# Kernel tuning notes

Hardware: AMD Instinct MI355X
Metric: run time of the kernel (lower is better)

The kernel has to match this reference:

```python
import jax, jax.numpy as jnp
import numpy as np

N = 100000   # nodes per type (author == paper count here)
E = 800000   # edges per edge type
D = 128      # input feature dim
HID = 128    # hidden_channels
OUT = 64     # out_channels
L = 2        # num_layers


def setup_inputs() -> dict:
    key = jax.random.key(0)
    ks = jax.random.split(key, 14)
    x_author = jax.random.normal(ks[0], (N, D), jnp.float32)
    x_paper = jax.random.normal(ks[1], (N, D), jnp.float32)
    edge_ap = jnp.stack([
        jax.random.randint(ks[2], (E,), 0, N),
        jax.random.randint(ks[3], (E,), 0, N),
    ]).astype(jnp.int32)  # [2,E] author->paper (src,dst)
    # paper->author: ensure every paper id appears as a source so the
    # meta-path conversion keeps all E edges (static shape under jit)
    pa_src = jnp.concatenate([jnp.arange(N), jax.random.randint(ks[4], (E - N,), 0, N)]).astype(jnp.int32)
    pa_dst = jax.random.randint(ks[5], (E,), 0, N).astype(jnp.int32)
    edge_pa = jnp.stack([pa_src, pa_dst])
    perm = jax.random.permutation(ks[6], N).astype(jnp.int32)  # DGI corruption
    s = 0.05
    # SAGEConv params: [layer, edge_type] with edge_type 0 = (author->paper), 1 = (paper->author)
    sage_Wl = jax.random.normal(ks[7], (L, 2, HID, D), jnp.float32) * s   # neighbor lin
    sage_Wr = jax.random.normal(ks[8], (L, 2, HID, D), jnp.float32) * s   # root lin
    sage_b = jnp.zeros((L, 2, HID), jnp.float32)
    # GATConv (heads=1) params
    gat_W = jax.random.normal(ks[9], (OUT, HID), jnp.float32) * s
    gat_att_src = jax.random.normal(ks[10], (OUT,), jnp.float32) * s
    gat_att_dst = jax.random.normal(ks[11], (OUT,), jnp.float32) * s
    gat_b = jnp.zeros((OUT,), jnp.float32)
    prelu_a = jnp.asarray(0.25, jnp.float32)
    return dict(x_author=x_author, x_paper=x_paper, sage_Wl=sage_Wl, sage_Wr=sage_Wr,
                sage_b=sage_b, gat_W=gat_W, gat_att_src=gat_att_src, gat_att_dst=gat_att_dst,
                gat_b=gat_b, prelu_a=prelu_a, edge_ap=edge_ap, edge_pa=edge_pa, perm=perm)


def _sage(x_src, x_dst, src, dst, Wl, Wr, b, n_dst):
    # SAGEConv: mean-aggregate neighbor feats, lin_l(agg) + lin_r(root) + bias
    agg = jax.ops.segment_sum(x_src[src], dst, num_segments=n_dst)       # [n_dst, D]
    cnt = jax.ops.segment_sum(jnp.ones((src.shape[0],), x_src.dtype), dst, num_segments=n_dst)
    mean = agg / jnp.maximum(cnt, 1.0)[:, None]
    return mean @ Wl.T + x_dst @ Wr.T + b


def _gat_prelu(feat, src, dst, W, a_src, a_dst, b, prelu_a, n):
    # GATConv heads=1 (self loops already appended by caller) + PReLU
    h = feat @ W.T                                                        # [n, OUT]
    e = jax.nn.leaky_relu((h @ a_src)[src] + (h @ a_dst)[dst], 0.2)       # [E']
    m = jax.ops.segment_max(e, dst, num_segments=n)
    ex = jnp.exp(e - m[dst])
    den = jax.ops.segment_sum(ex, dst, num_segments=n)
    coef = ex / den[dst]
    out = jax.ops.segment_sum(coef[:, None] * h[src], dst, num_segments=n) + b
    return jnp.where(out >= 0, out, prelu_a * out)


def reference(x_author, x_paper, sage_Wl, sage_Wr, sage_b, gat_W, gat_att_src,
              gat_att_dst, gat_b, prelu_a, edge_ap, edge_pa, perm):
    # Original loop feeds xx_dict into every layer, so only the LAST layer's
    # output survives; and only x_dict['author'] is consumed downstream.
    l = L - 1
    h_author = jax.nn.leaky_relu(
        _sage(x_paper, x_author, edge_pa[0], edge_pa[1],
              sage_Wl[l, 1], sage_Wr[l, 1], sage_b[l, 1], N), 0.01)
    # meta-path author->author edges (paper mapped via last-write paper->author dict)
    p2a = jnp.zeros((N,), jnp.int32).at[edge_pa[0]].set(edge_pa[1])
    self_loop = jnp.arange(N, dtype=jnp.int32)  # GATConv add_self_loops=True
    meta_src = jnp.concatenate([edge_ap[0], self_loop])
    meta_dst = jnp.concatenate([p2a[edge_ap[1]], self_loop])
    pos = _gat_prelu(h_author, meta_src, meta_dst, gat_W, gat_att_src, gat_att_dst, gat_b, prelu_a, N)
    neg = _gat_prelu(h_author[perm], meta_src, meta_dst, gat_W, gat_att_src, gat_att_dst, gat_b, prelu_a, N)
    summary = jnp.mean(pos, axis=0)
    return pos, neg, summary
```

## Files before the change

kernel.cpp:

```cpp
#include <hip/hip_runtime.h>
#include <stdint.h>

#define NN 100000
#define EE 800000
#define DD 128
#define HH 128
#define OO 64

#define SPA 40
#define SME 112

#define PREP_EDGE_B  3125
#define PREP_CASTX_B 12500
#define PREP_CASTW_B 40
#define P2_SAGE_B    25000
#define P2_CMP_B     391
#define P3_GEMM_B    782
#define P3_META_B    3125

typedef __attribute__((ext_vector_type(8))) short short8v;
typedef __attribute__((ext_vector_type(4))) float f32x4;

__device__ __forceinline__ unsigned short f2bf(float f) {
    union { float f; unsigned int u; } v; v.f = f;
    unsigned int u = v.u;
    u = (u + 0x7fffu + ((u >> 16) & 1u)) >> 16;
    return (unsigned short)u;
}
__device__ __forceinline__ float bf2f(unsigned short b) {
    union { unsigned int u; float f; } v; v.u = ((unsigned int)b) << 16;
    return v.f;
}

__global__ __launch_bounds__(256) void k_prep(const int* __restrict__ pa_src,
                                              const int* __restrict__ pa_dst,
                                              const float* __restrict__ x,
                                              const float* __restrict__ Wl,
                                              const float* __restrict__ Wr,
                                              const float* __restrict__ Wg,
                                              int* __restrict__ amax,
                                              int* __restrict__ cnt_pa,
                                              int* __restrict__ col_pa,
                                              unsigned short* __restrict__ xbf,
                                              unsigned short* __restrict__ wbf) {
    int b = blockIdx.x, t = threadIdx.x;
    if (b < PREP_EDGE_B) {
        int e = b * 256 + t;
        if (e >= EE) return;
        int s = pa_src[e], d = pa_dst[e];
        atomicMax(&amax[s], e);
        int pos = atomicAdd(&cnt_pa[d], 1);
        if (pos < SPA) __builtin_nontemporal_store(s, &col_pa[d * SPA + pos]);
    } else if (b < PREP_EDGE_B + PREP_CASTX_B) {
        long i = (long)(b - PREP_EDGE_B) * 256 + t;
        if (i >= (long)NN * DD / 4) return;
        float4 v = ((const float4*)x)[i];
        ushort4 w;
        w.x = f2bf(v.x); w.y = f2bf(v.y); w.z = f2bf(v.z); w.w = f2bf(v.w);
        ((ushort4*)xbf)[i] = w;
    } else {
        int i4 = (b - PREP_EDGE_B - PREP_CASTX_B) * 256 + t;
        if (i4 >= 10240) return;
        float4 v;
        if (i4 < 4096)       v = ((const float4*)Wl)[i4];
        else if (i4 < 8192)  v = ((const float4*)Wr)[i4 - 4096];
        else                 v = ((const float4*)Wg)[i4 - 8192];
        ushort4 w;
        w.x = f2bf(v.x); w.y = f2bf(v.y); w.z = f2bf(v.z); w.w = f2bf(v.w);
        ((ushort4*)wbf)[i4] = w;
    }
}

__global__ __launch_bounds__(256) void k_pack2(const int* __restrict__ cnt_pa,
                                               const int* __restrict__ col_pa,
                                               const unsigned short* __restrict__ xbf,
                                               const int* __restrict__ amax,
                                               const int* __restrict__ pa_dst,
                                               int* __restrict__ p2a32,
                                               unsigned short* __restrict__ mean_bf) {
    int b = blockIdx.x, t = threadIdx.x;
    if (b < P2_SAGE_B) {
        long gid = (long)b * 256 + t;
        int d = (int)(gid >> 6);
        if (d >= NN) return;
        int lane = (int)(gid & 63);
        int dcnt = cnt_pa[d];
        int deg = (dcnt > SPA) ? SPA : dcnt;
        const int* row = col_pa + d * SPA;
        float ax = 0.f, ay = 0.f;
        int i = 0;
        for (; i + 3 < deg; i += 4) {
            int s0 = row[i], s1 = row[i + 1], s2 = row[i + 2], s3 = row[i + 3];
            ushort2 v0 = ((const ushort2*)(xbf + (long)s0 * DD))[lane];
            ushort2 v1 = ((const ushort2*)(xbf + (long)s1 * DD))[lane];
            ushort2 v2 = ((const ushort2*)(xbf + (long)s2 * DD))[lane];
            ushort2 v3 = ((const ushort2*)(xbf + (long)s3 * DD))[lane];
            ax += (bf2f(v0.x) + bf2f(v1.x)) + (bf2f(v2.x) + bf2f(v3.x));
            ay += (bf2f(v0.y) + bf2f(v1.y)) + (bf2f(v2.y) + bf2f(v3.y));
        }
        for (; i < deg; ++i) {
            int s = row[i];
            ushort2 v = ((const ushort2*)(xbf + (long)s * DD))[lane];
            ax += bf2f(v.x);
            ay += bf2f(v.y);
        }
        float sc = 1.0f / fmaxf((float)dcnt, 1.0f);
        ushort2 w;
        w.x = f2bf(ax * sc);
        w.y = f2bf(ay * sc);
        ((ushort2*)(mean_bf + (long)d * DD))[lane] = w;
    } else {
        int s = (b - P2_SAGE_B) * 256 + t;
        if (s >= NN) return;
        p2a32[s] = pa_dst[amax[s]];
    }
}

__global__ __launch_bounds__(256) void k_pack3(const unsigned short* __restrict__ mean_bf,
                                               const float* __restrict__ xa,
                                               const unsigned short* __restrict__ wbf,
                                               const float* __restrict__ sb,
                                               const float* __restrict__ asrc,
                                               const float* __restrict__ adst,
                                               unsigned short* __restrict__ hg,
                                               float* __restrict__ al_s,
                                               float* __restrict__ al_d,
                                               const int* __restrict__ ap_src,
                                               const int* __restrict__ ap_dst,
                                               const int* __restrict__ p2a32,
                                               int* __restrict__ cnt_meta,
                                               int* __restrict__ col_meta) {
    __shared__ unsigned short hs[4 * 32 * 128];
    int b = blockIdx.x, t = threadIdx.x;
    if (b >= P3_GEMM_B) {
        int e = (b - P3_GEMM_B) * 256 + t;
        if (e >= EE) return;
        int d = p2a32[ap_dst[e]];
        int pos = atomicAdd(&cnt_meta[d], 1);
        if (pos < SME) __builtin_nontemporal_store(ap_src[e], &col_meta[d * SME + pos]);
        return;
    }
    const unsigned short* wl = wbf;
    const unsigned short* wr = wbf + 16384;
    const unsigned short* wg = wbf + 32768;
    int wave = t >> 6, lane = t & 63;
    int rowbase = b * 128 + wave * 32;
    int lr = lane & 15;
    int q = lane >> 4;
    int kq = q * 8;
    int r0 = rowbase + lr, r1 = r0 + 16;
    int cr0 = (r0 < NN) ? r0 : 0;
    int cr1 = (r1 < NN) ? r1 : 0;

    f32x4 acc[2][8];
    #pragma unroll
    for (int i = 0; i < 2; ++i)
        #pragma unroll
        for (int j = 0; j < 8; ++j) { f32x4 z = {0.f,0.f,0.f,0.f}; acc[i][j] = z; }

    #pragma unroll
    for (int k0 = 0; k0 < DD; k0 += 32) {
        int kk = k0 + kq;
        short8v am0 = *(const short8v*)(mean_bf + (long)cr0 * DD + kk);
        short8v am1 = *(const short8v*)(mean_bf + (long)cr1 * DD + kk);
        const float4* q0 = (const float4*)(xa + (long)cr0 * DD + kk);
        const float4* q1 = (const float4*)(xa + (long)cr1 * DD + kk);
        float4 a0 = q0[0], b0 = q0[1], a1 = q1[0], b1 = q1[1];
        short8v ax0, ax1;
        ax0[0]=(short)f2bf(a0.x); ax0[1]=(short)f2bf(a0.y); ax0[2]=(short)f2bf(a0.z); ax0[3]=(short)f2bf(a0.w);
        ax0[4]=(short)f2bf(b0.x); ax0[5]=(short)f2bf(b0.y); ax0[6]=(short)f2bf(b0.z); ax0[7]=(short)f2bf(b0.w);
        ax1[0]=(short)f2bf(a1.x); ax1[1]=(short)f2bf(a1.y); ax1[2]=(short)f2bf(a1.z); ax1[3]=(short)f2bf(a1.w);
        ax1[4]=(short)f2bf(b1.x); ax1[5]=(short)f2bf(b1.y); ax1[6]=(short)f2bf(b1.z); ax1[7]=(short)f2bf(b1.w);
        #pragma unroll
        for (int nb = 0; nb < 8; ++nb) {
            int o = nb * 16 + lr;
            short8v bl = *(const short8v*)(wl + o * DD + kk);
            short8v br = *(const short8v*)(wr + o * DD + kk);
            acc[0][nb] = __builtin_amdgcn_mfma_f32_16x16x32_bf16(am0, bl, acc[0][nb], 0, 0, 0);
            acc[1][nb] = __builtin_amdgcn_mfma_f32_16x16x32_bf16(am1, bl, acc[1][nb], 0, 0, 0);
            acc[0][nb] = __builtin_amdgcn_mfma_f32_16x16x32_bf16(ax0, br, acc[0][nb], 0, 0, 0);
            acc[1][nb] = __builtin_amdgcn_mfma_f32_16x16x32_bf16(ax1, br, acc[1][nb], 0, 0, 0);
        }
    }
    char* hbase = (char*)hs + wave * 8192;
    #pragma unroll
    for (int rh = 0; rh < 2; ++rh) {
        #pragma unroll
        for (int nb = 0; nb < 8; ++nb) {
            int col = nb * 16 + lr;
            float bias = sb[col];
            #pragma unroll
            for (int r = 0; r < 4; ++r) {
                int lrow = rh * 16 + q * 4 + r;
                float v = acc[rh][nb][r] + bias;
                v = (v >= 0.f) ? v : 0.01f * v;
                int boff = (lrow * 256 + col * 2) ^ ((lrow & 7) << 4);
                *(unsigned short*)(hbase + boff) = f2bf(v);
            }
        }
    }
    f32x4 acc2[2][4];
    #pragma unroll
    for (int i = 0; i < 2; ++i)
        #pragma unroll
        for (int j = 0; j < 4; ++j) { f32x4 z = {0.f,0.f,0.f,0.f}; acc2[i][j] = z; }

    #pragma unroll
    for (int k0 = 0; k0 < HH; k0 += 32) {
        int kk = k0 + kq;
        int boff0 = (lr * 256 + kk * 2) ^ ((lr & 7) << 4);
        int boff1 = ((16 + lr) * 256 + kk * 2) ^ ((lr & 7) << 4);
        short8v a0 = *(const short8v*)(hbase + boff0);
        short8v a1 = *(const short8v*)(hbase + boff1);
        #pragma unroll
        for (int nb = 0; nb < 4; ++nb) {
            short8v bg = *(const short8v*)(wg + (nb * 16 + lr) * HH + kk);
            acc2[0][nb] = __builtin_amdgcn_mfma_f32_16x16x32_bf16(a0, bg, acc2[0][nb], 0, 0, 0);
            acc2[1][nb] = __builtin_amdgcn_mfma_f32_16x16x32_bf16(a1, bg, acc2[1][nb], 0, 0, 0);
        }
    }
    float a_s[4], a_d[4];
    #pragma unroll
    for (int nb = 0; nb < 4; ++nb) { a_s[nb] = asrc[nb * 16 + lr]; a_d[nb] = adst[nb * 16 + lr]; }
    #pragma unroll
    for (int rh = 0; rh < 2; ++rh) {
        float ss[4] = {0.f,0.f,0.f,0.f}, dd[4] = {0.f,0.f,0.f,0.f};
        #pragma unroll
        for (int nb = 0; nb < 4; ++nb) {
            #pragma unroll
            for (int r = 0; r < 4; ++r) {
                int row = rowbase + rh * 16 + q * 4 + r;
                unsigned short wb = f2bf(acc2[rh][nb][r]);
                if (row < NN) hg[(long)row * OO + nb * 16 + lr] = wb;
                float w = bf2f(wb);
                ss[r] += w * a_s[nb];
                dd[r] += w * a_d[nb];
            }
        }
        #pragma unroll
        for (int r = 0; r < 4; ++r) {
            float s = ss[r], dv = dd[r];
            #pragma unroll
            for (int off = 1; off < 16; off <<= 1) {
                s  += __shfl_xor(s,  off, 64);
                dv += __shfl_xor(dv, off, 64);
            }
            int row = rowbase + rh * 16 + q * 4 + r;
            if (lr == 0 && row < NN) { al_s[row] = s; al_d[row] = dv; }
        }
    }
}

__global__ __launch_bounds__(256) void k_gat_gather(const int* __restrict__ cnt_meta,
                                                    const int* __restrict__ col_meta,
                                                    const int* __restrict__ perm,
                                                    const float* __restrict__ al_s,
                                                    const float* __restrict__ al_d,
                                                    const unsigned short* __restrict__ hg,
                                                    const float* __restrict__ gb,
                                                    const float* __restrict__ prelu_a,
                                                    float* __restrict__ out) {
    long gid = (long)blockIdx.x * 256 + threadIdx.x;
    int d = (int)(gid >> 6);
    if (d >= NN) return;
    int j = (int)(gid & 63);
    int deg = cnt_meta[d];
    if (deg > SME) deg = SME;
    const int* row = col_meta + d * SME;
    int pd = perm[d];
    float add = al_d[d];
    float adn = al_d[pd];
    float lp = al_s[d] + add;   lp = (lp >= 0.f) ? lp : 0.2f * lp;
    float ln = al_s[pd] + adn;  ln = (ln >= 0.f) ? ln : 0.2f * ln;
    float xps = __expf(lp), xns = __expf(ln);
    float denp = xps, denn = xns;
    float accp = xps * bf2f(hg[((long)d << 6) + j]);
    float accn = xns * bf2f(hg[((long)pd << 6) + j]);

    for (int base = 0; base < deg; base += 64) {
        int cnt = deg - base;
        if (cnt > 64) cnt = 64;
        int s = 0, ps = 0;
        float xp = 0.f, xn = 0.f;
        if (j < cnt) {
            s = row[base + j];
            ps = perm[s];
            float l0 = al_s[s] + add;   l0 = (l0 >= 0.f) ? l0 : 0.2f * l0;
            xp = __expf(l0);
            float m0 = al_s[ps] + adn;  m0 = (m0 >= 0.f) ? m0 : 0.2f * m0;
            xn = __expf(m0);
        }
        float tp = xp, tn = xn;
        #pragma unroll
        for (int off = 32; off; off >>= 1) {
            tp += __shfl_xor(tp, off, 64);
            tn += __shfl_xor(tn, off, 64);
        }
        denp += tp;
        denn += tn;
        int e = 0;
        for (; e + 3 < cnt; e += 4) {
            int s0 = __shfl(s, e),   s1 = __shfl(s, e + 1),   s2 = __shfl(s, e + 2),   s3 = __shfl(s, e + 3);
            int p0 = __shfl(ps, e),  p1 = __shfl(ps, e + 1),  p2 = __shfl(ps, e + 2),  p3 = __shfl(ps, e + 3);
            float a0 = __shfl(xp, e), a1 = __shfl(xp, e + 1), a2 = __shfl(xp, e + 2), a3 = __shfl(xp, e + 3);
            float b0 = __shfl(xn, e), b1 = __shfl(xn, e + 1), b2 = __shfl(xn, e + 2), b3 = __shfl(xn, e + 3);
            float h0 = bf2f(hg[((long)s0 << 6) + j]);
            float h1 = bf2f(hg[((long)s1 << 6) + j]);
            float h2 = bf2f(hg[((long)s2 << 6) + j]);
            float h3 = bf2f(hg[((long)s3 << 6) + j]);
            float g0 = bf2f(hg[((long)p0 << 6) + j]);
            float g1 = bf2f(hg[((long)p1 << 6) + j]);
            float g2 = bf2f(hg[((long)p2 << 6) + j]);
            float g3 = bf2f(hg[((long)p3 << 6) + j]);
            accp += (a0 * h0 + a1 * h1) + (a2 * h2 + a3 * h3);
            accn += (b0 * g0 + b1 * g1) + (b2 * g2 + b3 * g3);
        }
        for (; e < cnt; ++e) {
            int sb2 = __shfl(s, e);
            int pb = __shfl(ps, e);
            float ab = __shfl(xp, e);
            float bb = __shfl(xn, e);
            accp += ab * bf2f(hg[((long)sb2 << 6) + j]);
            accn += bb * bf2f(hg[((long)pb << 6) + j]);
        }
    }
    float bias = gb[j];
    float a = prelu_a[0];
    float vp = accp / denp + bias;
    vp = (vp >= 0.f) ? vp : a * vp;
    out[((long)d << 6) + j] = vp;
    float vn = accn / denn + bias;
    vn = (vn >= 0.f) ? vn : a * vn;
    out[((long)(NN + d) << 6) + j] = vn;
}

__global__ __launch_bounds__(256) void k_summary(const float* __restrict__ out_pos,
                                                 float* __restrict__ summary) {
    int t = threadIdx.x;
    int j = t & 63, sub = t >> 6;
    float acc = 0.f;
    for (int row = blockIdx.x * 4 + sub; row < NN; row += 256 * 4) {
        acc += out_pos[(long)row * OO + j];
    }
    __shared__ float red[4][OO];
    red[sub][j] = acc;
    __syncthreads();
    if (sub == 0) {
        float ttl = red[0][j] + red[1][j] + red[2][j] + red[3][j];
        atomicAdd(summary + j, ttl * (1.0f / NN));
    }
}

extern "C" void kernel_launch(void* const* d_in, const int* in_sizes, int n_in,
                              void* d_out, int out_size, void* d_ws, size_t ws_size,
                              hipStream_t stream) {
    const float* x_author = (const float*)d_in[0];
    const float* x_paper  = (const float*)d_in[1];
    const float* sage_Wl  = (const float*)d_in[2];
    const float* sage_Wr  = (const float*)d_in[3];
    const float* sage_b   = (const float*)d_in[4];
    const float* gat_W    = (const float*)d_in[5];
    const float* gat_as   = (const float*)d_in[6];
    const float* gat_ad   = (const float*)d_in[7];
    const float* gat_b    = (const float*)d_in[8];
    const float* prelu_a  = (const float*)d_in[9];
    const int*   edge_ap  = (const int*)d_in[10];
    const int*   edge_pa  = (const int*)d_in[11];
    const int*   perm     = (const int*)d_in[12];

    char* ws = (char*)d_ws;
    int*   cnt_pa    = (int*)(ws + 0);
    int*   cnt_meta  = (int*)(ws + 400000);
    int*   amax      = (int*)(ws + 800000);
    int*   p2a32     = (int*)(ws + 1200000);
    float* al_s      = (float*)(ws + 1600000);
    float* al_d      = (float*)(ws + 2000000);
    unsigned short* wbf = (unsigned short*)(ws + 2400000);
    int*   col_pa    = (int*)(ws + 2481920);
    unsigned short* mean_bf = (unsigned short*)(ws + 18481920);
    unsigned short* xbf     = (unsigned short*)(ws + 44081920);
    int*   col_meta  = (int*)(ws + 44081920);
    unsigned short* hg = (unsigned short*)col_pa;

    hipMemsetAsync(d_ws, 0, 1200000, stream);
    hipMemsetAsync((char*)d_out + (size_t)2 * NN * OO * sizeof(float), 0,
                   OO * sizeof(float), stream);

    const float* Wl = sage_Wl + 3 * HH * DD;
    const float* Wr = sage_Wr + 3 * HH * DD;
    const float* sb = sage_b  + 3 * HH;

    k_prep<<<PREP_EDGE_B + PREP_CASTX_B + PREP_CASTW_B, 256, 0, stream>>>(
        edge_pa, edge_pa + EE, x_paper, Wl, Wr, gat_W, amax, cnt_pa, col_pa, xbf, wbf);
    k_pack2<<<P2_SAGE_B + P2_CMP_B, 256, 0, stream>>>(
        cnt_pa, col_pa, xbf, amax, edge_pa + EE, p2a32, mean_bf);
    k_pack3<<<P3_GEMM_B + P3_META_B, 256, 0, stream>>>(
        mean_bf, x_author, wbf, sb, gat_as, gat_ad, hg, al_s, al_d,
        edge_ap, edge_ap + EE, p2a32, cnt_meta, col_meta);
    k_gat_gather<<<(NN * 64 + 255) / 256, 256, 0, stream>>>(cnt_meta, col_meta, perm,
                                                            al_s, al_d, hg, gat_b, prelu_a,
                                                            (float*)d_out);
    k_summary<<<256, 256, 0, stream>>>((float*)d_out, (float*)d_out + 2L * NN * OO);
}
```

Measured before the change: 339.4 us.

## Replace materialized meta-path CSR with two-level author-paper adjacency walk

Rather than building a bucketed author->author meta-path adjacency with atomics after the paper->author map exists, the edges are bucketed by paper in the prep kernel, in parallel with the paper->author bucketing. The pack kernel then builds an inverse map from each author to the papers that resolve to it. The GAT gather walks those papers and their author lists. This removes the 800k-edge atomic scatter that sat in the GEMM kernel and lets the GEMM run alone. The cost is a nested loop in the gather that handles only about 8 edges per 64-lane pass, which leaves many lanes idle, and extra workspace memory.

```diff
diff --git a/kernel.cpp b/kernel.cpp
--- a/kernel.cpp
+++ b/kernel.cpp
@@ -8,15 +8,15 @@
 #define OO 64
 
 #define SPA 40
-#define SME 112
-
-#define PREP_EDGE_B  3125
+#define SAP 40
+#define SIV 24
+
+#define PREP_PAIR_B  6250
 #define PREP_CASTX_B 12500
 #define PREP_CASTW_B 40
 #define P2_SAGE_B    25000
-#define P2_CMP_B     391
-#define P3_GEMM_B    782
-#define P3_META_B    3125
+#define P2_INV_B     391
+#define GEMM_B       782
 
 typedef __attribute__((ext_vector_type(8))) short short8v;
 typedef __attribute__((ext_vector_type(4))) float f32x4;
@@ -34,6 +34,8 @@
 
 __global__ __launch_bounds__(256) void k_prep(const int* __restrict__ pa_src,
                                               const int* __restrict__ pa_dst,
+                                              const int* __restrict__ ap_src,
+                                              const int* __restrict__ ap_dst,
                                               const float* __restrict__ x,
                                               const float* __restrict__ Wl,
                                               const float* __restrict__ Wr,
@@ -41,25 +43,33 @@
                                               int* __restrict__ amax,
                                               int* __restrict__ cnt_pa,
                                               int* __restrict__ col_pa,
+                                              int* __restrict__ cnt_ap,
+                                              int* __restrict__ col_ap,
                                               unsigned short* __restrict__ xbf,
                                               unsigned short* __restrict__ wbf) {
     int b = blockIdx.x, t = threadIdx.x;
-    if (b < PREP_EDGE_B) {
-        int e = b * 256 + t;
+    if (b < PREP_PAIR_B) {
+        int e = (b >> 1) * 256 + t;
         if (e >= EE) return;
-        int s = pa_src[e], d = pa_dst[e];
-        atomicMax(&amax[s], e);
-        int pos = atomicAdd(&cnt_pa[d], 1);
-        if (pos < SPA) __builtin_nontemporal_store(s, &col_pa[d * SPA + pos]);
-    } else if (b < PREP_EDGE_B + PREP_CASTX_B) {
-        long i = (long)(b - PREP_EDGE_B) * 256 + t;
+        if ((b & 1) == 0) {
+            int s = pa_src[e], d = pa_dst[e];
+            atomicMax(&amax[s], e);
+            int pos = atomicAdd(&cnt_pa[d], 1);
+            if (pos < SPA) __builtin_nontemporal_store(s, &col_pa[d * SPA + pos]);
+        } else {
+            int s = ap_src[e], p = ap_dst[e];
+            int pos = atomicAdd(&cnt_ap[p], 1);
+            if (pos < SAP) __builtin_nontemporal_store(s, &col_ap[p * SAP + pos]);
+        }
+    } else if (b < PREP_PAIR_B + PREP_CASTX_B) {
+        long i = (long)(b - PREP_PAIR_B) * 256 + t;
         if (i >= (long)NN * DD / 4) return;
         float4 v = ((const float4*)x)[i];
         ushort4 w;
         w.x = f2bf(v.x); w.y = f2bf(v.y); w.z = f2bf(v.z); w.w = f2bf(v.w);
         ((ushort4*)xbf)[i] = w;
     } else {
-        int i4 = (b - PREP_EDGE_B - PREP_CASTX_B) * 256 + t;
+        int i4 = (b - PREP_PAIR_B - PREP_CASTX_B) * 256 + t;
         if (i4 >= 10240) return;
         float4 v;
         if (i4 < 4096)       v = ((const float4*)Wl)[i4];
@@ -76,7 +86,8 @@
                                                const unsigned short* __restrict__ xbf,
                                                const int* __restrict__ amax,
                                                const int* __restrict__ pa_dst,
-                                               int* __restrict__ p2a32,
+                                               int* __restrict__ cnt_inv,
+                                               int* __restrict__ col_inv,
                                                unsigned short* __restrict__ mean_bf) {
     int b = blockIdx.x, t = threadIdx.x;
     if (b < P2_SAGE_B) {
@@ -110,36 +121,25 @@
         w.y = f2bf(ay * sc);
         ((ushort2*)(mean_bf + (long)d * DD))[lane] = w;
     } else {
-        int s = (b - P2_SAGE_B) * 256 + t;
-        if (s >= NN) return;
-        p2a32[s] = pa_dst[amax[s]];
-    }
-}
-
-__global__ __launch_bounds__(256) void k_pack3(const unsigned short* __restrict__ mean_bf,
-                                               const float* __restrict__ xa,
-                                               const unsigned short* __restrict__ wbf,
-                                               const float* __restrict__ sb,
-                                               const float* __restrict__ asrc,
-                                               const float* __restrict__ adst,
-                                               unsigned short* __restrict__ hg,
-                                               float* __restrict__ al_s,
-                                               float* __restrict__ al_d,
-                                               const int* __restrict__ ap_src,
-                                               const int* __restrict__ ap_dst,
-                                               const int* __restrict__ p2a32,
-                                               int* __restrict__ cnt_meta,
-                                               int* __restrict__ col_meta) {
+        int p = (b - P2_SAGE_B) * 256 + t;
+        if (p >= NN) return;
+        int d = pa_dst[amax[p]];
+        int pos = atomicAdd(&cnt_inv[d], 1);
+        if (pos < SIV) col_inv[d * SIV + pos] = p;
+    }
+}
+
+__global__ __launch_bounds__(256) void k_gemm(const unsigned short* __restrict__ mean_bf,
+                                              const float* __restrict__ xa,
+                                              const unsigned short* __restrict__ wbf,
+                                              const float* __restrict__ sb,
+                                              const float* __restrict__ asrc,
+                                              const float* __restrict__ adst,
+                                              unsigned short* __restrict__ hg,
+                                              float* __restrict__ al_s,
+                                              float* __restrict__ al_d) {
     __shared__ unsigned short hs[4 * 32 * 128];
     int b = blockIdx.x, t = threadIdx.x;
-    if (b >= P3_GEMM_B) {
-        int e = (b - P3_GEMM_B) * 256 + t;
-        if (e >= EE) return;
-        int d = p2a32[ap_dst[e]];
-        int pos = atomicAdd(&cnt_meta[d], 1);
-        if (pos < SME) __builtin_nontemporal_store(ap_src[e], &col_meta[d * SME + pos]);
-        return;
-    }
     const unsigned short* wl = wbf;
     const unsigned short* wr = wbf + 16384;
     const unsigned short* wg = wbf + 32768;
@@ -251,8 +251,10 @@
     }
 }
 
-__global__ __launch_bounds__(256) void k_gat_gather(const int* __restrict__ cnt_meta,
-                                                    const int* __restrict__ col_meta,
+__global__ __launch_bounds__(256) void k_gat_gather(const int* __restrict__ cnt_inv,
+                                                    const int* __restrict__ col_inv,
+                                                    const int* __restrict__ cnt_ap,
+                                                    const int* __restrict__ col_ap,
                                                     const int* __restrict__ perm,
                                                     const float* __restrict__ al_s,
                                                     const float* __restrict__ al_d,
@@ -264,9 +266,8 @@
     int d = (int)(gid >> 6);
     if (d >= NN) return;
     int j = (int)(gid & 63);
-    int deg = cnt_meta[d];
-    if (deg > SME) deg = SME;
-    const int* row = col_meta + d * SME;
+    int npap = cnt_inv[d];
+    if (npap > SIV) npap = SIV;
     int pd = perm[d];
     float add = al_d[d];
     float adn = al_d[pd];
@@ -277,13 +278,15 @@
     float accp = xps * bf2f(hg[((long)d << 6) + j]);
     float accn = xns * bf2f(hg[((long)pd << 6) + j]);
 
-    for (int base = 0; base < deg; base += 64) {
-        int cnt = deg - base;
-        if (cnt > 64) cnt = 64;
+    for (int ip = 0; ip < npap; ++ip) {
+        int p = col_inv[d * SIV + ip];
+        int na = cnt_ap[p];
+        if (na > SAP) na = SAP;
+        const int* arow = col_ap + p * SAP;
         int s = 0, ps = 0;
         float xp = 0.f, xn = 0.f;
-        if (j < cnt) {
-            s = row[base + j];
+        if (j < na) {
+            s = arow[j];
             ps = perm[s];
             float l0 = al_s[s] + add;   l0 = (l0 >= 0.f) ? l0 : 0.2f * l0;
             xp = __expf(l0);
@@ -299,7 +302,7 @@
         denp += tp;
         denn += tn;
         int e = 0;
-        for (; e + 3 < cnt; e += 4) {
+        for (; e + 3 < na; e += 4) {
             int s0 = __shfl(s, e),   s1 = __shfl(s, e + 1),   s2 = __shfl(s, e + 2),   s3 = __shfl(s, e + 3);
             int p0 = __shfl(ps, e),  p1 = __shfl(ps, e + 1),  p2 = __shfl(ps, e + 2),  p3 = __shfl(ps, e + 3);
             float a0 = __shfl(xp, e), a1 = __shfl(xp, e + 1), a2 = __shfl(xp, e + 2), a3 = __shfl(xp, e + 3);
@@ -315,7 +318,7 @@
             accp += (a0 * h0 + a1 * h1) + (a2 * h2 + a3 * h3);
             accn += (b0 * g0 + b1 * g1) + (b2 * g2 + b3 * g3);
         }
-        for (; e < cnt; ++e) {
+        for (; e < na; ++e) {
             int sb2 = __shfl(s, e);
             int pb = __shfl(ps, e);
             float ab = __shfl(xp, e);
@@ -370,19 +373,20 @@
 
     char* ws = (char*)d_ws;
     int*   cnt_pa    = (int*)(ws + 0);
-    int*   cnt_meta  = (int*)(ws + 400000);
-    int*   amax      = (int*)(ws + 800000);
-    int*   p2a32     = (int*)(ws + 1200000);
+    int*   cnt_ap    = (int*)(ws + 400000);
+    int*   cnt_inv   = (int*)(ws + 800000);
+    int*   amax      = (int*)(ws + 1200000);
     float* al_s      = (float*)(ws + 1600000);
     float* al_d      = (float*)(ws + 2000000);
     unsigned short* wbf = (unsigned short*)(ws + 2400000);
     int*   col_pa    = (int*)(ws + 2481920);
-    unsigned short* mean_bf = (unsigned short*)(ws + 18481920);
+    int*   col_ap    = (int*)(ws + 18481920);
+    int*   col_inv   = (int*)(ws + 34481920);
     unsigned short* xbf     = (unsigned short*)(ws + 44081920);
-    int*   col_meta  = (int*)(ws + 44081920);
+    unsigned short* mean_bf = (unsigned short*)(ws + 69681920);
     unsigned short* hg = (unsigned short*)col_pa;
 
-    hipMemsetAsync(d_ws, 0, 1200000, stream);
+    hipMemsetAsync(d_ws, 0, 1600000, stream);
     hipMemsetAsync((char*)d_out + (size_t)2 * NN * OO * sizeof(float), 0,
                    OO * sizeof(float), stream);
 
@@ -390,15 +394,15 @@
     const float* Wr = sage_Wr + 3 * HH * DD;
     const float* sb = sage_b  + 3 * HH;
 
-    k_prep<<<PREP_EDGE_B + PREP_CASTX_B + PREP_CASTW_B, 256, 0, stream>>>(
-        edge_pa, edge_pa + EE, x_paper, Wl, Wr, gat_W, amax, cnt_pa, col_pa, xbf, wbf);
-    k_pack2<<<P2_SAGE_B + P2_CMP_B, 256, 0, stream>>>(
-        cnt_pa, col_pa, xbf, amax, edge_pa + EE, p2a32, mean_bf);
-    k_pack3<<<P3_GEMM_B + P3_META_B, 256, 0, stream>>>(
-        mean_bf, x_author, wbf, sb, gat_as, gat_ad, hg, al_s, al_d,
-        edge_ap, edge_ap + EE, p2a32, cnt_meta, col_meta);
-    k_gat_gather<<<(NN * 64 + 255) / 256, 256, 0, stream>>>(cnt_meta, col_meta, perm,
-                                                            al_s, al_d, hg, gat_b, prelu_a,
+    k_prep<<<PREP_PAIR_B + PREP_CASTX_B + PREP_CASTW_B, 256, 0, stream>>>(
+        edge_pa, edge_pa + EE, edge_ap, edge_ap + EE, x_paper, Wl, Wr, gat_W,
+        amax, cnt_pa, col_pa, cnt_ap, col_ap, xbf, wbf);
+    k_pack2<<<P2_SAGE_B + P2_INV_B, 256, 0, stream>>>(
+        cnt_pa, col_pa, xbf, amax, edge_pa + EE, cnt_inv, col_inv, mean_bf);
+    k_gemm<<<GEMM_B, 256, 0, stream>>>(mean_bf, x_author, wbf, sb, gat_as, gat_ad,
+                                       hg, al_s, al_d);
+    k_gat_gather<<<(NN * 64 + 255) / 256, 256, 0, stream>>>(cnt_inv, col_inv, cnt_ap, col_ap,
+                                                            perm, al_s, al_d, hg, gat_b, prelu_a,
                                                             (float*)d_out);
     k_summary<<<256, 256, 0, stream>>>((float*)d_out, (float*)d_out + 2L * NN * OO);
 }
```

New measurement: 410.3 us. 1.21x slower.

## Drop p2a buffer and interleave meta-edge build with SAGE gather

Applied to the files above, without the earlier changes.

Removes the intermediate p2a32 array: the meta-edge bucketing now resolves the paper-to-author mapping inline via pa_dst[amax[p]]. When the workspace is large enough, col_meta gets its own region so the meta bucketing can run in the same launch as the SAGE mean gather, with one meta block interleaved every 9 blocks. The GEMM then runs alone in its own kernel. The aim is to overlap the atomic-heavy meta build with the bandwidth-bound gather and shorten the GEMM launch. The cost is an extra dependent load per edge and a path that depends on workspace size.

```diff
diff --git a/kernel.cpp b/kernel.cpp
--- a/kernel.cpp
+++ b/kernel.cpp
@@ -13,10 +13,9 @@
 #define PREP_EDGE_B  3125
 #define PREP_CASTX_B 12500
 #define PREP_CASTW_B 40
-#define P2_SAGE_B    25000
-#define P2_CMP_B     391
-#define P3_GEMM_B    782
-#define P3_META_B    3125
+#define SAGE_B       25000
+#define META_B       3125
+#define GEMM_B       782
 
 typedef __attribute__((ext_vector_type(8))) short short8v;
 typedef __attribute__((ext_vector_type(4))) float f32x4;
@@ -30,6 +29,55 @@
 __device__ __forceinline__ float bf2f(unsigned short b) {
     union { unsigned int u; float f; } v; v.u = ((unsigned int)b) << 16;
     return v.f;
+}
+
+__device__ __forceinline__ void sage_body(long gid,
+                                          const int* __restrict__ cnt_pa,
+                                          const int* __restrict__ col_pa,
+                                          const unsigned short* __restrict__ xbf,
+                                          unsigned short* __restrict__ mean_bf) {
+    int d = (int)(gid >> 6);
+    if (d >= NN) return;
+    int lane = (int)(gid & 63);
+    int dcnt = cnt_pa[d];
+    int deg = (dcnt > SPA) ? SPA : dcnt;
+    const int* row = col_pa + d * SPA;
+    float ax = 0.f, ay = 0.f;
+    int i = 0;
+    for (; i + 3 < deg; i += 4) {
+        int s0 = row[i], s1 = row[i + 1], s2 = row[i + 2], s3 = row[i + 3];
+        ushort2 v0 = ((const ushort2*)(xbf + (long)s0 * DD))[lane];
+        ushort2 v1 = ((const ushort2*)(xbf + (long)s1 * DD))[lane];
+        ushort2 v2 = ((const ushort2*)(xbf + (long)s2 * DD))[lane];
+        ushort2 v3 = ((const ushort2*)(xbf + (long)s3 * DD))[lane];
+        ax += (bf2f(v0.x) + bf2f(v1.x)) + (bf2f(v2.x) + bf2f(v3.x));
+        ay += (bf2f(v0.y) + bf2f(v1.y)) + (bf2f(v2.y) + bf2f(v3.y));
+    }
+    for (; i < deg; ++i) {
+        int s = row[i];
+        ushort2 v = ((const ushort2*)(xbf + (long)s * DD))[lane];
+        ax += bf2f(v.x);
+        ay += bf2f(v.y);
+    }
+    float sc = 1.0f / fmaxf((float)dcnt, 1.0f);
+    ushort2 w;
+    w.x = f2bf(ax * sc);
+    w.y = f2bf(ay * sc);
+    ((ushort2*)(mean_bf + (long)d * DD))[lane] = w;
+}
+
+__device__ __forceinline__ void meta_body(int e,
+                                          const int* __restrict__ ap_src,
+                                          const int* __restrict__ ap_dst,
+                                          const int* __restrict__ amax,
+                                          const int* __restrict__ pa_dst,
+                                          int* __restrict__ cnt_meta,
+                                          int* __restrict__ col_meta) {
+    if (e >= EE) return;
+    int p = ap_dst[e];
+    int d = pa_dst[amax[p]];
+    int pos = atomicAdd(&cnt_meta[d], 1);
+    if (pos < SME) __builtin_nontemporal_store(ap_src[e], &col_meta[d * SME + pos]);
 }
 
 __global__ __launch_bounds__(256) void k_prep(const int* __restrict__ pa_src,
@@ -71,75 +119,43 @@
     }
 }
 
-__global__ __launch_bounds__(256) void k_pack2(const int* __restrict__ cnt_pa,
-                                               const int* __restrict__ col_pa,
-                                               const unsigned short* __restrict__ xbf,
-                                               const int* __restrict__ amax,
-                                               const int* __restrict__ pa_dst,
-                                               int* __restrict__ p2a32,
-                                               unsigned short* __restrict__ mean_bf) {
+__global__ __launch_bounds__(256) void k_pack2a(const int* __restrict__ cnt_pa,
+                                                const int* __restrict__ col_pa,
+                                                const unsigned short* __restrict__ xbf,
+                                                unsigned short* __restrict__ mean_bf,
+                                                const int* __restrict__ ap_src,
+                                                const int* __restrict__ ap_dst,
+                                                const int* __restrict__ amax,
+                                                const int* __restrict__ pa_dst,
+                                                int* __restrict__ cnt_meta,
+                                                int* __restrict__ col_meta) {
     int b = blockIdx.x, t = threadIdx.x;
-    if (b < P2_SAGE_B) {
-        long gid = (long)b * 256 + t;
-        int d = (int)(gid >> 6);
-        if (d >= NN) return;
-        int lane = (int)(gid & 63);
-        int dcnt = cnt_pa[d];
-        int deg = (dcnt > SPA) ? SPA : dcnt;
-        const int* row = col_pa + d * SPA;
-        float ax = 0.f, ay = 0.f;
-        int i = 0;
-        for (; i + 3 < deg; i += 4) {
-            int s0 = row[i], s1 = row[i + 1], s2 = row[i + 2], s3 = row[i + 3];
-            ushort2 v0 = ((const ushort2*)(xbf + (long)s0 * DD))[lane];
-            ushort2 v1 = ((const ushort2*)(xbf + (long)s1 * DD))[lane];
-            ushort2 v2 = ((const ushort2*)(xbf + (long)s2 * DD))[lane];
-            ushort2 v3 = ((const ushort2*)(xbf + (long)s3 * DD))[lane];
-            ax += (bf2f(v0.x) + bf2f(v1.x)) + (bf2f(v2.x) + bf2f(v3.x));
-            ay += (bf2f(v0.y) + bf2f(v1.y)) + (bf2f(v2.y) + bf2f(v3.y));
-        }
-        for (; i < deg; ++i) {
-            int s = row[i];
-            ushort2 v = ((const ushort2*)(xbf + (long)s * DD))[lane];
-            ax += bf2f(v.x);
-            ay += bf2f(v.y);
-        }
-        float sc = 1.0f / fmaxf((float)dcnt, 1.0f);
-        ushort2 w;
-        w.x = f2bf(ax * sc);
-        w.y = f2bf(ay * sc);
-        ((ushort2*)(mean_bf + (long)d * DD))[lane] = w;
+    if (b % 9 == 0) {
+        int mb = b / 9;
+        meta_body(mb * 256 + t, ap_src, ap_dst, amax, pa_dst, cnt_meta, col_meta);
     } else {
-        int s = (b - P2_SAGE_B) * 256 + t;
-        if (s >= NN) return;
-        p2a32[s] = pa_dst[amax[s]];
-    }
-}
-
-__global__ __launch_bounds__(256) void k_pack3(const unsigned short* __restrict__ mean_bf,
-                                               const float* __restrict__ xa,
-                                               const unsigned short* __restrict__ wbf,
-                                               const float* __restrict__ sb,
-                                               const float* __restrict__ asrc,
-                                               const float* __restrict__ adst,
-                                               unsigned short* __restrict__ hg,
-                                               float* __restrict__ al_s,
-                                               float* __restrict__ al_d,
-                                               const int* __restrict__ ap_src,
-                                               const int* __restrict__ ap_dst,
-                                               const int* __restrict__ p2a32,
-                                               int* __restrict__ cnt_meta,
-                                               int* __restrict__ col_meta) {
-    __shared__ unsigned short hs[4 * 32 * 128];
-    int b = blockIdx.x, t = threadIdx.x;
-    if (b >= P3_GEMM_B) {
-        int e = (b - P3_GEMM_B) * 256 + t;
-        if (e >= EE) return;
-        int d = p2a32[ap_dst[e]];
-        int pos = atomicAdd(&cnt_meta[d], 1);
-        if (pos < SME) __builtin_nontemporal_store(ap_src[e], &col_meta[d * SME + pos]);
-        return;
-    }
+        long sb = b - b / 9 - 1;
+        sage_body(sb * 256 + t, cnt_pa, col_pa, xbf, mean_bf);
+    }
+}
+
+__global__ __launch_bounds__(256) void k_pack2b(const int* __restrict__ cnt_pa,
+                                                const int* __restrict__ col_pa,
+                                                const unsigned short* __restrict__ xbf,
+                                                unsigned short* __restrict__ mean_bf) {
+    sage_body((long)blockIdx.x * 256 + threadIdx.x, cnt_pa, col_pa, xbf, mean_bf);
+}
+
+__device__ __forceinline__ void gemm_body(int b, int t, unsigned short* hs,
+                                          const unsigned short* __restrict__ mean_bf,
+                                          const float* __restrict__ xa,
+                                          const unsigned short* __restrict__ wbf,
+                                          const float* __restrict__ sb,
+                                          const float* __restrict__ asrc,
+                                          const float* __restrict__ adst,
+                                          unsigned short* __restrict__ hg,
+                                          float* __restrict__ al_s,
+                                          float* __restrict__ al_d) {
     const unsigned short* wl = wbf;
     const unsigned short* wr = wbf + 16384;
     const unsigned short* wg = wbf + 32768;
@@ -249,6 +265,43 @@
             if (lr == 0 && row < NN) { al_s[row] = s; al_d[row] = dv; }
         }
     }
+}
+
+__global__ __launch_bounds__(256) void k_gemm(const unsigned short* __restrict__ mean_bf,
+                                              const float* __restrict__ xa,
+                                              const unsigned short* __restrict__ wbf,
+                                              const float* __restrict__ sb,
+                                              const float* __restrict__ asrc,
+                                              const float* __restrict__ adst,
+                                              unsigned short* __restrict__ hg,
+                                              float* __restrict__ al_s,
+                                              float* __restrict__ al_d) {
+    __shared__ unsigned short hs[4 * 32 * 128];
+    gemm_body(blockIdx.x, threadIdx.x, hs, mean_bf, xa, wbf, sb, asrc, adst, hg, al_s, al_d);
+}
+
+__global__ __launch_bounds__(256) void k_pack3b(const unsigned short* __restrict__ mean_bf,
+                                                const float* __restrict__ xa,
+                                                const unsigned short* __restrict__ wbf,
+                                                const float* __restrict__ sb,
+                                                const float* __restrict__ asrc,
+                                                const float* __restrict__ adst,
+                                                unsigned short* __restrict__ hg,
+                                                float* __restrict__ al_s,
+                                                float* __restrict__ al_d,
+                                                const int* __restrict__ ap_src,
+                                                const int* __restrict__ ap_dst,
+                                                const int* __restrict__ amax,
+                                                const int* __restrict__ pa_dst,
+                                                int* __restrict__ cnt_meta,
+                                                int* __restrict__ col_meta) {
+    __shared__ unsigned short hs[4 * 32 * 128];
+    int b = blockIdx.x, t = threadIdx.x;
+    if (b >= GEMM_B) {
+        meta_body((b - GEMM_B) * 256 + t, ap_src, ap_dst, amax, pa_dst, cnt_meta, col_meta);
+        return;
+    }
+    gemm_body(b, t, hs, mean_bf, xa, wbf, sb, asrc, adst, hg, al_s, al_d);
 }
 
 __global__ __launch_bounds__(256) void k_gat_gather(const int* __restrict__ cnt_meta,
@@ -372,14 +425,24 @@
     int*   cnt_pa    = (int*)(ws + 0);
     int*   cnt_meta  = (int*)(ws + 400000);
     int*   amax      = (int*)(ws + 800000);
-    int*   p2a32     = (int*)(ws + 1200000);
-    float* al_s      = (float*)(ws + 1600000);
-    float* al_d      = (float*)(ws + 2000000);
-    unsigned short* wbf = (unsigned short*)(ws + 2400000);
-    int*   col_pa    = (int*)(ws + 2481920);
-    unsigned short* mean_bf = (unsigned short*)(ws + 18481920);
-    unsigned short* xbf     = (unsigned short*)(ws + 44081920);
-    int*   col_meta  = (int*)(ws + 44081920);
+    float* al_s      = (float*)(ws + 1200000);
+    float* al_d      = (float*)(ws + 1600000);
+    unsigned short* wbf = (unsigned short*)(ws + 2000000);
+    int*   col_pa    = (int*)(ws + 2081920);
+
+    const int pathA = (ws_size >= (size_t)114081920);
+    unsigned short* xbf;
+    unsigned short* mean_bf;
+    int* col_meta;
+    if (pathA) {
+        xbf      = (unsigned short*)(ws + 18081920);
+        mean_bf  = (unsigned short*)(ws + 43681920);
+        col_meta = (int*)(ws + 69281920);
+    } else {
+        mean_bf  = (unsigned short*)(ws + 18081920);
+        xbf      = (unsigned short*)(ws + 43681920);
+        col_meta = (int*)(ws + 43681920);
+    }
     unsigned short* hg = (unsigned short*)col_pa;
 
     hipMemsetAsync(d_ws, 0, 1200000, stream);
@@ -392,11 +455,18 @@
 
     k_prep<<<PREP_EDGE_B + PREP_CASTX_B + PREP_CASTW_B, 256, 0, stream>>>(
         edge_pa, edge_pa + EE, x_paper, Wl, Wr, gat_W, amax, cnt_pa, col_pa, xbf, wbf);
-    k_pack2<<<P2_SAGE_B + P2_CMP_B, 256, 0, stream>>>(
-        cnt_pa, col_pa, xbf, amax, edge_pa + EE, p2a32, mean_bf);
-    k_pack3<<<P3_GEMM_B + P3_META_B, 256, 0, stream>>>(
-        mean_bf, x_author, wbf, sb, gat_as, gat_ad, hg, al_s, al_d,
-        edge_ap, edge_ap + EE, p2a32, cnt_meta, col_meta);
+    if (pathA) {
+        k_pack2a<<<SAGE_B + META_B, 256, 0, stream>>>(
+            cnt_pa, col_pa, xbf, mean_bf,
+            edge_ap, edge_ap + EE, amax, edge_pa + EE, cnt_meta, col_meta);
+        k_gemm<<<GEMM_B, 256, 0, stream>>>(mean_bf, x_author, wbf, sb, gat_as, gat_ad,
+                                           hg, al_s, al_d);
+    } else {
+        k_pack2b<<<SAGE_B, 256, 0, stream>>>(cnt_pa, col_pa, xbf, mean_bf);
+        k_pack3b<<<GEMM_B + META_B, 256, 0, stream>>>(
+            mean_bf, x_author, wbf, sb, gat_as, gat_ad, hg, al_s, al_d,
+            edge_ap, edge_ap + EE, amax, edge_pa + EE, cnt_meta, col_meta);
+    }
     k_gat_gather<<<(NN * 64 + 255) / 256, 256, 0, stream>>>(cnt_meta, col_meta, perm,
                                                             al_s, al_d, hg, gat_b, prelu_a,
                                                             (float*)d_out);
```

New measurement: 342.7 us. About the same (+1.0%).
